# Kernel tuning notes

Hardware: AMD Instinct MI355X
Metric: run time of the kernel (lower is better)

## Reference

```python
import jax, jax.numpy as jnp
import numpy as np

B, N, C, IN, H, G, OUT = 128, 256, 4, 64, 128, 8, 1
NUM_GNN_LAYERS = 2  # num_layers - 1


def setup_inputs() -> dict:
    key = jax.random.key(0)
    k1, k2, k3, k4, k5, k6 = jax.random.split(key, 6)
    V = jax.random.normal(k1, (B, N, IN), dtype=jnp.float32)
    A = jax.random.uniform(k2, (B, N, C, N), dtype=jnp.float32)
    mol_size = jax.random.randint(k3, (B,), 16, N + 1)  # at least 16 real nodes
    W_in = jax.random.normal(k4, (2, H, IN, G), dtype=jnp.float32) / np.float32(np.sqrt(IN) * np.sqrt(G))
    W_g = jax.random.normal(k5, (NUM_GNN_LAYERS, 2, H, H, G), dtype=jnp.float32) / np.float32(np.sqrt(H) * np.sqrt(G))
    W_out = jax.random.normal(k6, (2, OUT, H, 1), dtype=jnp.float32) / np.float32(np.sqrt(H))
    b_out = jnp.zeros((1, OUT), dtype=jnp.float32)
    return {"V": V, "A": A, "mol_size": mol_size, "W_in": W_in, "W_g": W_g, "W_out": W_out, "b_out": b_out}


def _kan_linear(x, W, bias=None):
    # x: [..., in], W: [2, out, in, grid]
    g = W.shape[-1]
    k = jnp.arange(1, g + 1, dtype=x.dtype)  # [g]
    xk = x[..., None] * k                    # [..., in, g]
    y = jnp.einsum('...ik,oik->...o', jnp.cos(xk), W[0]) \
      + jnp.einsum('...ik,oik->...o', jnp.sin(xk), W[1])
    if bias is not None:
        y = y + bias
    return y


def _kan_gnn_layer(h, A, W):
    # h: [b,n,in], A: [b,n,c,m], W: [2,out,in,grid]
    g = W.shape[-1]
    k = jnp.arange(1, g + 1, dtype=h.dtype)
    xk = h[..., None] * k                      # [b,n,in,g]
    f = jnp.einsum('bnik,oik->bno', jnp.cos(xk), W[0]) \
      + jnp.einsum('bnik,oik->bno', jnp.sin(xk), W[1])  # fourier_feat [b,n,out]
    # torch chain permute/reshape/bmm/sum(c) == sum_{n,c} A[b,n,c,m] * f[b,n,o]
    return jnp.einsum('bncm,bno->bmo', A, f)   # [b,m,out]


def reference(V, A, mol_size, W_in, W_g, W_out, b_out):
    h = _kan_linear(V, W_in)                   # [B,N,H]
    for i in range(W_g.shape[0]):
        m = _kan_gnn_layer(h, A, W_g[i])
        h = jax.nn.leaky_relu(m + h, negative_slope=0.01)
    # avg pooling over the first mol_size[i] (real) nodes per graph
    node_mask = (jnp.arange(N) < mol_size[:, None]).astype(h.dtype)  # [B,N]
    summed = jnp.einsum('bnh,bn->bh', h, node_mask)
    y = summed / mol_size[:, None].astype(h.dtype)                    # [B,H]
    out = jax.nn.sigmoid(_kan_linear(y, W_out, b_out))                # [B,OUT]
    return out
```

## Files before the change

kernel.cpp:

```cpp
#include <hip/hip_runtime.h>
#include <math.h>

namespace {
constexpr int B_ = 128;
constexpr int N_ = 256;
constexpr int H_ = 128;
constexpr int M_TOTAL = B_ * N_;
}

#define AS1 __attribute__((address_space(1)))
#define AS3 __attribute__((address_space(3)))

__device__ __forceinline__ void gl_lds16(const float* g, float* l) {
  __builtin_amdgcn_global_load_lds((const AS1 unsigned int*)g,
                                   (AS3 unsigned int*)l, 16, 0, 0);
}

template<int I, int O>
__global__ __launch_bounds__(256)
void wtr_kernel(const float* __restrict__ in, float* __restrict__ out) {
  int idx = blockIdx.x * 256 + threadIdx.x;
  constexpr int TOTAL = 2 * O * I * 8;
  if (idx >= TOTAL) return;
  int g = idx & 7;
  int t = idx >> 3;
  int i = t % I;
  int t2 = t / I;
  int o = t2 % O;
  int s = t2 / O;
  out[(size_t)((i * 8 + g) * 2 + s) * O + o] = in[idx];
}

template<int IN>
__global__ __launch_bounds__(256, 4)
void fourier8(const float* __restrict__ x,
              const float* __restrict__ Wt,
              float* __restrict__ out)
{
  constexpr int CHUNKS = IN / 2;
  __shared__ alignas(16) float wl[2][16][2][128];
  __shared__ alignas(16) float fC[2][16][64];
  __shared__ alignas(16) float fS[2][16][64];

  const int tid = threadIdx.x;
  const int node0 = blockIdx.x * 64;
  const int og = tid & 15;
  const int ng = tid >> 4;
  const int lane = tid & 63;
  const int wave = tid >> 6;
  const int fnode = tid & 63;
  const int fil = wave >> 1;
  const int fhi = wave & 1;

  const float* xrow = x + (size_t)(node0 + fnode) * IN;

  float acc[4][8];
  #pragma unroll
  for (int a = 0; a < 4; ++a)
    #pragma unroll
    for (int b = 0; b < 8; ++b) acc[a][b] = 0.f;

  auto put_feats = [&](int pb, float xx) {
    float s1, c1;
    sincosf(xx, &s1, &c1);
    float ck, sk;
    if (fhi == 0) {
      ck = c1; sk = s1;
    } else {
      float c2 = c1 * c1 - s1 * s1, s2 = 2.f * c1 * s1;
      float c4 = c2 * c2 - s2 * s2, s4 = 2.f * s2 * c2;
      ck = c4 * c1 - s4 * s1;
      sk = s4 * c1 + c4 * s1;
    }
    const int r0 = fil * 8 + fhi * 4;
    #pragma unroll
    for (int t = 0; t < 4; ++t) {
      fC[pb][r0 + t][fnode] = ck;
      fS[pb][r0 + t][fnode] = sk;
      float cn = ck * c1 - sk * s1;
      sk = sk * c1 + ck * s1;
      ck = cn;
    }
  };

  auto stage_w = [&](int pb, int ic) {
    const float* wsrc = Wt + (size_t)ic * 4096;
    float* wdst = &wl[pb][0][0][0];
    #pragma unroll
    for (int q = 0; q < 4; ++q) {
      gl_lds16(wsrc + (size_t)(q * 256 + tid) * 4,
               wdst + (size_t)(q * 1024 + wave * 256) + 0);
    }
  };

  stage_w(0, 0);
  float xv = xrow[fil];
  float xn = (CHUNKS > 1) ? xrow[2 + fil] : 0.f;
  put_feats(0, xv);
  __syncthreads();

  int p = 0;
  for (int ic = 0; ic < CHUNKS; ++ic) {
    const int pn = p ^ 1;
    if (ic + 1 < CHUNKS) stage_w(pn, ic + 1);
    float xn2 = (ic + 2 < CHUNKS) ? xrow[2 * (ic + 2) + fil] : 0.f;
    #pragma unroll 2
    for (int j = 0; j < 16; ++j) {
      float4 fc = *(const float4*)&fC[p][j][ng * 4];
      float4 fs = *(const float4*)&fS[p][j][ng * 4];
      float4 w0a = *(const float4*)&wl[p][j][0][og * 4];
      float4 w0b = *(const float4*)&wl[p][j][0][og * 4 + 64];
      float4 w1a = *(const float4*)&wl[p][j][1][og * 4];
      float4 w1b = *(const float4*)&wl[p][j][1][og * 4 + 64];
      float fcv[4] = {fc.x, fc.y, fc.z, fc.w};
      float fsv[4] = {fs.x, fs.y, fs.z, fs.w};
      float wa0[4] = {w0a.x, w0a.y, w0a.z, w0a.w};
      float wb0[4] = {w0b.x, w0b.y, w0b.z, w0b.w};
      float wa1[4] = {w1a.x, w1a.y, w1a.z, w1a.w};
      float wb1[4] = {w1b.x, w1b.y, w1b.z, w1b.w};
      #pragma unroll
      for (int nd = 0; nd < 4; ++nd) {
        #pragma unroll
        for (int oo = 0; oo < 4; ++oo) {
          acc[nd][oo]     += fcv[nd] * wa0[oo] + fsv[nd] * wa1[oo];
          acc[nd][4 + oo] += fcv[nd] * wb0[oo] + fsv[nd] * wb1[oo];
        }
      }
    }
    if (ic + 1 < CHUNKS) put_feats(pn, xn);
    xn = xn2;
    __syncthreads();
    p ^= 1;
  }

  #pragma unroll
  for (int nd = 0; nd < 4; ++nd) {
    int row = node0 + ng * 4 + nd;
    float4 ra = {acc[nd][0], acc[nd][1], acc[nd][2], acc[nd][3]};
    float4 rb = {acc[nd][4], acc[nd][5], acc[nd][6], acc[nd][7]};
    *(float4*)&out[(size_t)row * H_ + og * 4] = ra;
    *(float4*)&out[(size_t)row * H_ + og * 4 + 64] = rb;
  }
}

__global__ __launch_bounds__(256)
void agg2(const float* __restrict__ A,
          const float* __restrict__ f,
          const float* __restrict__ h_in,
          float* __restrict__ h_out)
{
  __shared__ alignas(16) float As[2][32][64];
  __shared__ alignas(16) float fsh[2][8][128];
  const int tid = threadIdx.x;
  const int b = blockIdx.x >> 2;
  const int m0 = (blockIdx.x & 3) * 64;
  const int og = tid & 15;
  const int mg = tid >> 4;
  const int wave = tid >> 6;

  float acc[4][8];
  #pragma unroll
  for (int i = 0; i < 4; ++i)
    #pragma unroll
    for (int j = 0; j < 8; ++j) acc[i][j] = 0.f;

  const float* Ab = A + (size_t)b * (N_ * 4 * N_) + m0;
  const float* fb = f + (size_t)b * (N_ * H_);

  #pragma unroll
  for (int q = 0; q < 2; ++q) {
    int v = q * 256 + tid;
    gl_lds16(Ab + (size_t)(v >> 4) * N_ + (v & 15) * 4,
             &As[0][0][0] + (size_t)(q * 256 + wave * 64) * 4);
  }
  gl_lds16(fb + (size_t)(tid >> 5) * H_ + (tid & 31) * 4,
           &fsh[0][0][0] + (size_t)(wave * 64) * 4);
  __syncthreads();

  int p = 0;
  for (int ch = 0; ch < 32; ++ch) {
    const int pn = p ^ 1;
    if (ch + 1 < 32) {
      const float* Asrc = Ab + (size_t)(ch + 1) * 32 * N_;
      #pragma unroll
      for (int q = 0; q < 2; ++q) {
        int v = q * 256 + tid;
        gl_lds16(Asrc + (size_t)(v >> 4) * N_ + (v & 15) * 4,
                 &As[pn][0][0] + (size_t)(q * 256 + wave * 64) * 4);
      }
      gl_lds16(fb + (size_t)((ch + 1) * 8 + (tid >> 5)) * H_ + (tid & 31) * 4,
               &fsh[pn][0][0] + (size_t)(wave * 64) * 4);
    }
    #pragma unroll
    for (int kk = 0; kk < 32; ++kk) {
      float4 a  = *(const float4*)&As[p][kk][mg * 4];
      float4 f0 = *(const float4*)&fsh[p][kk >> 2][og * 4];
      float4 f1 = *(const float4*)&fsh[p][kk >> 2][og * 4 + 64];
      float av[4] = {a.x, a.y, a.z, a.w};
      float fo[8] = {f0.x, f0.y, f0.z, f0.w, f1.x, f1.y, f1.z, f1.w};
      #pragma unroll
      for (int mi = 0; mi < 4; ++mi)
        #pragma unroll
        for (int oi = 0; oi < 8; ++oi)
          acc[mi][oi] += av[mi] * fo[oi];
    }
    __syncthreads();
    p ^= 1;
  }

  #pragma unroll
  for (int mi = 0; mi < 4; ++mi) {
    int row = b * N_ + m0 + mg * 4 + mi;
    const float* hr = &h_in[(size_t)row * H_];
    float* ho = &h_out[(size_t)row * H_];
    float4 r0 = *(const float4*)&hr[og * 4];
    float4 r1 = *(const float4*)&hr[og * 4 + 64];
    float4 o0, o1;
    float v;
    v = acc[mi][0] + r0.x; o0.x = v >= 0.f ? v : 0.01f * v;
    v = acc[mi][1] + r0.y; o0.y = v >= 0.f ? v : 0.01f * v;
    v = acc[mi][2] + r0.z; o0.z = v >= 0.f ? v : 0.01f * v;
    v = acc[mi][3] + r0.w; o0.w = v >= 0.f ? v : 0.01f * v;
    v = acc[mi][4] + r1.x; o1.x = v >= 0.f ? v : 0.01f * v;
    v = acc[mi][5] + r1.y; o1.y = v >= 0.f ? v : 0.01f * v;
    v = acc[mi][6] + r1.z; o1.z = v >= 0.f ? v : 0.01f * v;
    v = acc[mi][7] + r1.w; o1.w = v >= 0.f ? v : 0.01f * v;
    *(float4*)&ho[og * 4] = o0;
    *(float4*)&ho[og * 4 + 64] = o1;
  }
}

__global__ __launch_bounds__(128)
void pool_kernel(const float* __restrict__ h,
                 const int* __restrict__ mol,
                 const float* __restrict__ Wout,
                 const float* __restrict__ bout,
                 float* __restrict__ out)
{
  __shared__ float red[128];
  const int b = blockIdx.x;
  const int t = threadIdx.x;
  const int ms = mol[b];
  const float* hb = h + (size_t)b * N_ * H_;
  float sum = 0.f;
  for (int n = 0; n < ms; ++n) sum += hb[(size_t)n * H_ + t];
  float y = sum / (float)ms;
  float s1, c1;
  sincosf(y, &s1, &c1);
  red[t] = c1 * Wout[t] + s1 * Wout[H_ + t];
  __syncthreads();
  for (int sft = 64; sft > 0; sft >>= 1) {
    if (t < sft) red[t] += red[t + sft];
    __syncthreads();
  }
  if (t == 0) {
    float z = red[0] + bout[0];
    out[b] = 1.f / (1.f + expf(-z));
  }
}

extern "C" void kernel_launch(void* const* d_in, const int* in_sizes, int n_in,
                              void* d_out, int out_size, void* d_ws, size_t ws_size,
                              hipStream_t stream) {
  const float* V    = (const float*)d_in[0];
  const float* A    = (const float*)d_in[1];
  const int*   mol  = (const int*)d_in[2];
  const float* Win  = (const float*)d_in[3];
  const float* Wg   = (const float*)d_in[4];
  const float* Wout = (const float*)d_in[5];
  const float* bout = (const float*)d_in[6];
  float* out = (float*)d_out;

  const size_t BUF = (size_t)M_TOTAL * H_;
  float* h     = (float*)d_ws;
  float* h2    = h  + BUF;
  float* f     = h2 + BUF;
  float* wt_in = f  + BUF;
  float* wt_g0 = wt_in + 512 * 2 * H_;
  float* wt_g1 = wt_g0 + 1024 * 2 * H_;

  wtr_kernel<64, 128><<<(2 * 128 * 64 * 8) / 256, 256, 0, stream>>>(Win, wt_in);
  wtr_kernel<128, 128><<<(2 * 128 * 128 * 8) / 256, 256, 0, stream>>>(Wg, wt_g0);
  wtr_kernel<128, 128><<<(2 * 128 * 128 * 8) / 256, 256, 0, stream>>>(
      Wg + (size_t)2 * 128 * 128 * 8, wt_g1);

  fourier8<64><<<M_TOTAL / 64, 256, 0, stream>>>(V, wt_in, h);

  float* hc = h;
  float* hn = h2;
  const float* wt_g[2] = {wt_g0, wt_g1};
  for (int l = 0; l < 2; ++l) {
    fourier8<128><<<M_TOTAL / 64, 256, 0, stream>>>(hc, wt_g[l], f);
    agg2<<<B_ * 4, 256, 0, stream>>>(A, f, hc, hn);
    float* tmp = hc; hc = hn; hn = tmp;
  }

  pool_kernel<<<B_, 128, 0, stream>>>(hc, mol, Wout, bout, out);
}
```

Measured before the change: 979.4 us.

## Compute Fourier features in registers per thread instead of staging through LDS

Each thread now computes the cos/sin features for its own four nodes in registers, using hardware sin/cos on a range-reduced argument and a rotation recurrence across the harmonics. This replaces the cooperative feature computation that wrote fC/fS into LDS. It removes the LDS feature traffic and half of the shared memory, and sets occupancy to 2 waves per EU. In exchange each thread recomputes features redundantly across the 16 output groups, and the fast sin/cos intrinsics plus the recurrence may reduce accuracy.

```diff
diff --git a/kernel.cpp b/kernel.cpp
--- a/kernel.cpp
+++ b/kernel.cpp
@@ -6,6 +6,7 @@
 constexpr int N_ = 256;
 constexpr int H_ = 128;
 constexpr int M_TOTAL = B_ * N_;
+constexpr float INV2PI = 0.15915494309189535f;
 }
 
 #define AS1 __attribute__((address_space(1)))
@@ -32,56 +33,28 @@
 }
 
 template<int IN>
-__global__ __launch_bounds__(256, 4)
-void fourier8(const float* __restrict__ x,
-              const float* __restrict__ Wt,
-              float* __restrict__ out)
+__global__ __launch_bounds__(256)
+__attribute__((amdgpu_waves_per_eu(2, 2)))
+void fourier12(const float* __restrict__ x,
+               const float* __restrict__ Wt,
+               float* __restrict__ out)
 {
   constexpr int CHUNKS = IN / 2;
   __shared__ alignas(16) float wl[2][16][2][128];
-  __shared__ alignas(16) float fC[2][16][64];
-  __shared__ alignas(16) float fS[2][16][64];
 
   const int tid = threadIdx.x;
   const int node0 = blockIdx.x * 64;
   const int og = tid & 15;
   const int ng = tid >> 4;
-  const int lane = tid & 63;
   const int wave = tid >> 6;
-  const int fnode = tid & 63;
-  const int fil = wave >> 1;
-  const int fhi = wave & 1;
-
-  const float* xrow = x + (size_t)(node0 + fnode) * IN;
+
+  const float* xp = x + (size_t)(node0 + ng * 4) * IN;
 
   float acc[4][8];
   #pragma unroll
   for (int a = 0; a < 4; ++a)
     #pragma unroll
     for (int b = 0; b < 8; ++b) acc[a][b] = 0.f;
-
-  auto put_feats = [&](int pb, float xx) {
-    float s1, c1;
-    sincosf(xx, &s1, &c1);
-    float ck, sk;
-    if (fhi == 0) {
-      ck = c1; sk = s1;
-    } else {
-      float c2 = c1 * c1 - s1 * s1, s2 = 2.f * c1 * s1;
-      float c4 = c2 * c2 - s2 * s2, s4 = 2.f * s2 * c2;
-      ck = c4 * c1 - s4 * s1;
-      sk = s4 * c1 + c4 * s1;
-    }
-    const int r0 = fil * 8 + fhi * 4;
-    #pragma unroll
-    for (int t = 0; t < 4; ++t) {
-      fC[pb][r0 + t][fnode] = ck;
-      fS[pb][r0 + t][fnode] = sk;
-      float cn = ck * c1 - sk * s1;
-      sk = sk * c1 + ck * s1;
-      ck = cn;
-    }
-  };
 
   auto stage_w = [&](int pb, int ic) {
     const float* wsrc = Wt + (size_t)ic * 4096;
@@ -89,46 +62,79 @@
     #pragma unroll
     for (int q = 0; q < 4; ++q) {
       gl_lds16(wsrc + (size_t)(q * 256 + tid) * 4,
-               wdst + (size_t)(q * 1024 + wave * 256) + 0);
+               wdst + (size_t)(q * 1024 + wave * 256));
     }
   };
 
+  float xv[2][4], xn[2][4];
+  #pragma unroll
+  for (int nd = 0; nd < 4; ++nd) {
+    xv[0][nd] = xp[(size_t)nd * IN + 0];
+    xv[1][nd] = xp[(size_t)nd * IN + 1];
+  }
   stage_w(0, 0);
-  float xv = xrow[fil];
-  float xn = (CHUNKS > 1) ? xrow[2 + fil] : 0.f;
-  put_feats(0, xv);
+  if (CHUNKS > 1) {
+    #pragma unroll
+    for (int nd = 0; nd < 4; ++nd) {
+      xn[0][nd] = xp[(size_t)nd * IN + 2];
+      xn[1][nd] = xp[(size_t)nd * IN + 3];
+    }
+  }
   __syncthreads();
 
   int p = 0;
   for (int ic = 0; ic < CHUNKS; ++ic) {
     const int pn = p ^ 1;
     if (ic + 1 < CHUNKS) stage_w(pn, ic + 1);
-    float xn2 = (ic + 2 < CHUNKS) ? xrow[2 * (ic + 2) + fil] : 0.f;
-    #pragma unroll 2
-    for (int j = 0; j < 16; ++j) {
-      float4 fc = *(const float4*)&fC[p][j][ng * 4];
-      float4 fs = *(const float4*)&fS[p][j][ng * 4];
-      float4 w0a = *(const float4*)&wl[p][j][0][og * 4];
-      float4 w0b = *(const float4*)&wl[p][j][0][og * 4 + 64];
-      float4 w1a = *(const float4*)&wl[p][j][1][og * 4];
-      float4 w1b = *(const float4*)&wl[p][j][1][og * 4 + 64];
-      float fcv[4] = {fc.x, fc.y, fc.z, fc.w};
-      float fsv[4] = {fs.x, fs.y, fs.z, fs.w};
-      float wa0[4] = {w0a.x, w0a.y, w0a.z, w0a.w};
-      float wb0[4] = {w0b.x, w0b.y, w0b.z, w0b.w};
-      float wa1[4] = {w1a.x, w1a.y, w1a.z, w1a.w};
-      float wb1[4] = {w1b.x, w1b.y, w1b.z, w1b.w};
+    #pragma unroll
+    for (int ii = 0; ii < 2; ++ii) {
+      float c1[4], s1[4], ck[4], sk[4];
       #pragma unroll
       for (int nd = 0; nd < 4; ++nd) {
+        float r = xv[ii][nd] * INV2PI;
+        float fr = r - floorf(r);
+        s1[nd] = __builtin_amdgcn_sinf(fr);
+        c1[nd] = __builtin_amdgcn_cosf(fr);
+        ck[nd] = c1[nd]; sk[nd] = s1[nd];
+      }
+      #pragma unroll 2
+      for (int j = 0; j < 8; ++j) {
+        const float* wg = &wl[p][ii * 8 + j][0][0];
+        float4 w0a = *(const float4*)(wg + og * 4);
+        float4 w0b = *(const float4*)(wg + og * 4 + 64);
+        float4 w1a = *(const float4*)(wg + 128 + og * 4);
+        float4 w1b = *(const float4*)(wg + 128 + og * 4 + 64);
+        float wc[8] = {w0a.x, w0a.y, w0a.z, w0a.w,
+                       w0b.x, w0b.y, w0b.z, w0b.w};
+        float ws[8] = {w1a.x, w1a.y, w1a.z, w1a.w,
+                       w1b.x, w1b.y, w1b.z, w1b.w};
         #pragma unroll
-        for (int oo = 0; oo < 4; ++oo) {
-          acc[nd][oo]     += fcv[nd] * wa0[oo] + fsv[nd] * wa1[oo];
-          acc[nd][4 + oo] += fcv[nd] * wb0[oo] + fsv[nd] * wb1[oo];
+        for (int nd = 0; nd < 4; ++nd) {
+          #pragma unroll
+          for (int oo = 0; oo < 8; ++oo)
+            acc[nd][oo] += ck[nd] * wc[oo] + sk[nd] * ws[oo];
+        }
+        if (j < 7) {
+          #pragma unroll
+          for (int nd = 0; nd < 4; ++nd) {
+            float cn = ck[nd] * c1[nd] - sk[nd] * s1[nd];
+            sk[nd] = sk[nd] * c1[nd] + ck[nd] * s1[nd];
+            ck[nd] = cn;
+          }
         }
       }
     }
-    if (ic + 1 < CHUNKS) put_feats(pn, xn);
-    xn = xn2;
+    #pragma unroll
+    for (int ii = 0; ii < 2; ++ii)
+      #pragma unroll
+      for (int nd = 0; nd < 4; ++nd) xv[ii][nd] = xn[ii][nd];
+    if (ic + 2 < CHUNKS) {
+      #pragma unroll
+      for (int nd = 0; nd < 4; ++nd) {
+        xn[0][nd] = xp[(size_t)nd * IN + (ic + 2) * 2];
+        xn[1][nd] = xp[(size_t)nd * IN + (ic + 2) * 2 + 1];
+      }
+    }
     __syncthreads();
     p ^= 1;
   }
@@ -284,13 +290,13 @@
   wtr_kernel<128, 128><<<(2 * 128 * 128 * 8) / 256, 256, 0, stream>>>(
       Wg + (size_t)2 * 128 * 128 * 8, wt_g1);
 
-  fourier8<64><<<M_TOTAL / 64, 256, 0, stream>>>(V, wt_in, h);
+  fourier12<64><<<M_TOTAL / 64, 256, 0, stream>>>(V, wt_in, h);
 
   float* hc = h;
   float* hn = h2;
   const float* wt_g[2] = {wt_g0, wt_g1};
   for (int l = 0; l < 2; ++l) {
-    fourier8<128><<<M_TOTAL / 64, 256, 0, stream>>>(hc, wt_g[l], f);
+    fourier12<128><<<M_TOTAL / 64, 256, 0, stream>>>(hc, wt_g[l], f);
     agg2<<<B_ * 4, 256, 0, stream>>>(A, f, hc, hn);
     float* tmp = hc; hc = hn; hn = tmp;
   }
```

After: 1.144 ms. 1.17x slower.
